# Performance work log

Measured on AMD Instinct MI355X. Metric: run time of the kernel, lower is better.

## Reference

```python
import jax, jax.numpy as jnp
import numpy as np

N_NODES = 100000
N_EDGES = 1600000
D = 64
HID = 512
N_CLASSES = 393


def gcn_conv(x, src, dst, W, b):
    """PyG-style GCNConv: h = x W; add self-loops; symmetric deg^-1/2 norm; scatter-add."""
    n = x.shape[0]
    h = x @ W  # [N, out]
    loop = jnp.arange(n)
    s = jnp.concatenate([src, loop])
    d = jnp.concatenate([dst, loop])
    deg = jax.ops.segment_sum(jnp.ones(d.shape[0], dtype=h.dtype), d, num_segments=n)
    dinv = jax.lax.rsqrt(jnp.maximum(deg, 1.0))  # self-loops guarantee deg >= 1
    norm = dinv[s] * dinv[d]  # [E+N]
    msg = h[s] * norm[:, None]  # [E+N, out] gather + scale
    out = jax.ops.segment_sum(msg, d, num_segments=n)  # scatter-add
    return out + b


def setup_inputs() -> dict:
    key = jax.random.key(0)
    ks = jax.random.split(key, 10)
    sc = 1.0 / np.sqrt(D)
    inp = {
        "adj": jax.random.randint(ks[0], (2, N_EDGES), 0, N_NODES, dtype=jnp.int64),
        "features": jax.random.normal(ks[1], (N_NODES, D), dtype=jnp.float32),
        "W1": jax.random.normal(ks[2], (D, D), dtype=jnp.float32) * sc,
        "b1": jnp.zeros((D,), jnp.float32),
        "W2": jax.random.normal(ks[3], (D, D), dtype=jnp.float32) * sc,
        "b2": jnp.zeros((D,), jnp.float32),
        "W3": jax.random.normal(ks[4], (D, D), dtype=jnp.float32) * sc,
        "b3": jnp.zeros((D,), jnp.float32),
        "Wlin": jax.random.normal(ks[5], (D, D), dtype=jnp.float32) * sc,
        "blin": jnp.zeros((D,), jnp.float32),
        "W4": jax.random.normal(ks[6], (N_NODES, HID), dtype=jnp.float32) / np.sqrt(N_NODES),
        "b4": jnp.zeros((HID,), jnp.float32),
        "W5": jax.random.normal(ks[7], (HID, N_CLASSES), dtype=jnp.float32) / np.sqrt(HID),
        "b5": jnp.zeros((N_CLASSES,), jnp.float32),
    }
    return inp


def reference(adj, features, W1, b1, W2, b2, W3, b3, Wlin, blin, W4, b4, W5, b5):
    src, dst = adj[0], adj[1]
    h = jax.nn.relu(gcn_conv(features, src, dst, W1, b1))
    h = jax.nn.relu(gcn_conv(h, src, dst, W2, b2))
    h = jax.nn.relu(gcn_conv(h, src, dst, W3, b3))
    scores = h @ Wlin + blin          # [N, 64]
    scores = scores.T                 # [64, N]
    scores = jax.nn.relu(scores @ W4 + b4)  # [64, HID]
    scores = scores @ W5 + b5         # [64, n_classes]
    return jax.nn.log_softmax(scores, axis=1)
```

## Files before the change

### kernel.cpp

```cpp
#include <hip/hip_runtime.h>
#include <math.h>

#define NN 100000
#define NE 1600000
#define HID 512
#define NCLS 393

__global__ void k_init(int* __restrict__ cnt, int* __restrict__ gtot) {
    int i = blockIdx.x * 256 + threadIdx.x;
    if (i < NN) cnt[i] = 0;
    if (i == 0) *gtot = 0;
}

__global__ void k_count(const int* __restrict__ dst, int* __restrict__ cnt) {
    int e = blockIdx.x * 256 + threadIdx.x;
    if (e < NE) atomicAdd(&cnt[dst[e]], 1);
}

__global__ void k_off(const int* __restrict__ cnt, float* __restrict__ dinv,
                      int* __restrict__ off, int* __restrict__ cur, int* __restrict__ gtot) {
    int i = blockIdx.x * 256 + threadIdx.x;
    if (i < NN) {
        int c = cnt[i];
        dinv[i] = rsqrtf(1.0f + (float)c);
        off[i] = atomicAdd(gtot, c);
        cur[i] = 0;
    }
}

__global__ void k_fill(const int* __restrict__ src, const int* __restrict__ dst,
                       const float* __restrict__ dinv, const int* __restrict__ off,
                       int* __restrict__ cur, int* __restrict__ eidx, float* __restrict__ enorm) {
    int e = blockIdx.x * 256 + threadIdx.x;
    if (e < NE) {
        int s = src[e], d = dst[e];
        int pos = off[d] + atomicAdd(&cur[d], 1);
        eidx[pos] = s;
        enorm[pos] = dinv[s] * dinv[d];
    }
}

template<bool IN_ACT, bool OUT_BIAS>
__global__ void k_gemm64b(const float* __restrict__ x, const float* __restrict__ W,
                          const float* __restrict__ bin, const float* __restrict__ bout,
                          float* __restrict__ out) {
    __shared__ float Ws[64 * 64];
    __shared__ float xs[32 * 64];
    int tid = threadIdx.x;
    size_t n0 = (size_t)blockIdx.x * 32;
    for (int i = tid; i < 1024; i += 256)
        ((float4*)Ws)[i] = ((const float4*)W)[i];
    for (int i = tid; i < 512; i += 256) {
        float4 v = ((const float4*)(x + n0 * 64))[i];
        if (IN_ACT) {
            int c = (i & 15) * 4;
            float4 bv = *(const float4*)(bin + c);
            v.x = fmaxf(v.x + bv.x, 0.f);
            v.y = fmaxf(v.y + bv.y, 0.f);
            v.z = fmaxf(v.z + bv.z, 0.f);
            v.w = fmaxf(v.w + bv.w, 0.f);
        }
        ((float4*)xs)[i] = v;
    }
    __syncthreads();
    int j = tid & 63, q = tid >> 6;
    float Wreg[64];
#pragma unroll
    for (int k = 0; k < 64; ++k) Wreg[k] = Ws[k * 64 + j];
    float bo = OUT_BIAS ? bout[j] : 0.f;
    for (int r = 0; r < 8; ++r) {
        int row = q * 8 + r;
        float acc = bo;
        const float4* xr = (const float4*)(xs + row * 64);
#pragma unroll
        for (int k4 = 0; k4 < 16; ++k4) {
            float4 xv = xr[k4];
            acc = fmaf(xv.x, Wreg[k4 * 4 + 0], acc);
            acc = fmaf(xv.y, Wreg[k4 * 4 + 1], acc);
            acc = fmaf(xv.z, Wreg[k4 * 4 + 2], acc);
            acc = fmaf(xv.w, Wreg[k4 * 4 + 3], acc);
        }
        out[(n0 + row) * 64 + j] = acc;
    }
}

__global__ void k_gather(const int* __restrict__ eidx, const float* __restrict__ enorm,
                         const int* __restrict__ off, const int* __restrict__ cnt,
                         const float* __restrict__ dinv, const float* __restrict__ t,
                         float* __restrict__ out) {
    int lane = threadIdx.x & 63;
    int n = (blockIdx.x * 256 + threadIdx.x) >> 6;
    if (n >= NN) return;
    float dv = dinv[n];
    float acc = t[(size_t)n * 64 + lane] * dv * dv;
    int o = off[n], c = cnt[n];
    for (int b = 0; b < c; b += 64) {
        int m = min(64, c - b);
        int sIdx = 0;
        float nrm = 0.f;
        if (lane < m) {
            sIdx = eidx[o + b + lane];
            nrm = enorm[o + b + lane];
        }
        int e = 0;
        for (; e + 4 <= m; e += 4) {
            int s0 = __shfl(sIdx, e + 0); float w0 = __shfl(nrm, e + 0);
            int s1 = __shfl(sIdx, e + 1); float w1 = __shfl(nrm, e + 1);
            int s2 = __shfl(sIdx, e + 2); float w2 = __shfl(nrm, e + 2);
            int s3 = __shfl(sIdx, e + 3); float w3 = __shfl(nrm, e + 3);
            float v0 = t[(size_t)s0 * 64 + lane];
            float v1 = t[(size_t)s1 * 64 + lane];
            float v2 = t[(size_t)s2 * 64 + lane];
            float v3 = t[(size_t)s3 * 64 + lane];
            acc = fmaf(v0, w0, acc);
            acc = fmaf(v1, w1, acc);
            acc = fmaf(v2, w2, acc);
            acc = fmaf(v3, w3, acc);
        }
        for (; e < m; ++e) {
            int s0 = __shfl(sIdx, e); float w0 = __shfl(nrm, e);
            acc = fmaf(t[(size_t)s0 * 64 + lane], w0, acc);
        }
    }
    out[(size_t)n * 64 + lane] = acc;
}

__global__ void k_zero(float* __restrict__ p, int n) {
    int i = blockIdx.x * 256 + threadIdx.x;
    if (i < n) p[i] = 0.f;
}

#define TG_KCHUNK 384
#define TG_NCH ((NN + TG_KCHUNK - 1) / TG_KCHUNK)
__global__ void k_tgemm2(const float* __restrict__ scores, const float* __restrict__ W4,
                         float* __restrict__ P) {
    __shared__ float ss[64 * 64];
    int colT = blockIdx.x & 3;
    int kch = blockIdx.x >> 2;
    int tid = threadIdx.x;
    int tc = tid & 31, tr = tid >> 5;
    int col = colT * 128 + tc * 4;
    float acc[8][4];
#pragma unroll
    for (int i = 0; i < 8; ++i)
#pragma unroll
        for (int c = 0; c < 4; ++c) acc[i][c] = 0.f;
    int k0 = kch * TG_KCHUNK;
    int k1 = min(k0 + TG_KCHUNK, NN);
    for (int kb = k0; kb < k1; kb += 64) {
        int cnt = min(64, k1 - kb);
        __syncthreads();
        for (int i = tid; i < 1024; i += 256) {
            float4 v = {0.f, 0.f, 0.f, 0.f};
            if ((i >> 4) < cnt) v = ((const float4*)(scores + (size_t)kb * 64))[i];
            ((float4*)ss)[i] = v;
        }
        __syncthreads();
        const float4* w4p = (const float4*)(W4 + (size_t)kb * 512 + col);
        for (int nIt = 0; nIt < cnt; ++nIt) {
            float4 w = w4p[(size_t)nIt * 128];
            const float4* sp = (const float4*)(ss + nIt * 64 + tr * 8);
            float4 s0 = sp[0], s1 = sp[1];
            float sarr[8] = {s0.x, s0.y, s0.z, s0.w, s1.x, s1.y, s1.z, s1.w};
#pragma unroll
            for (int i = 0; i < 8; ++i) {
                acc[i][0] = fmaf(sarr[i], w.x, acc[i][0]);
                acc[i][1] = fmaf(sarr[i], w.y, acc[i][1]);
                acc[i][2] = fmaf(sarr[i], w.z, acc[i][2]);
                acc[i][3] = fmaf(sarr[i], w.w, acc[i][3]);
            }
        }
    }
#pragma unroll
    for (int i = 0; i < 8; ++i) {
        int row = tr * 8 + i;
#pragma unroll
        for (int c = 0; c < 4; ++c)
            atomicAdd(&P[row * 512 + col + c], acc[i][c]);
    }
}

__global__ void k_final(const float* __restrict__ P, const float* __restrict__ b4,
                        const float* __restrict__ W5, const float* __restrict__ b5,
                        float* __restrict__ out) {
    __shared__ float p[HID];
    __shared__ float z[NCLS];
    __shared__ float red[256];
    int i = blockIdx.x;
    int tid = threadIdx.x;
    for (int k = tid; k < HID; k += 256) p[k] = fmaxf(P[i * HID + k] + b4[k], 0.f);
    __syncthreads();
    for (int c = tid; c < NCLS; c += 256) {
        float acc = b5[c];
        for (int k = 0; k < HID; ++k) acc = fmaf(p[k], W5[(size_t)k * NCLS + c], acc);
        z[c] = acc;
    }
    __syncthreads();
    float m = -INFINITY;
    for (int c = tid; c < NCLS; c += 256) m = fmaxf(m, z[c]);
    red[tid] = m;
    __syncthreads();
    for (int s = 128; s > 0; s >>= 1) {
        if (tid < s) red[tid] = fmaxf(red[tid], red[tid + s]);
        __syncthreads();
    }
    m = red[0];
    __syncthreads();
    float sum = 0.f;
    for (int c = tid; c < NCLS; c += 256) sum += expf(z[c] - m);
    red[tid] = sum;
    __syncthreads();
    for (int s = 128; s > 0; s >>= 1) {
        if (tid < s) red[tid] += red[tid + s];
        __syncthreads();
    }
    float lse = m + logf(red[0]);
    for (int c = tid; c < NCLS; c += 256) out[i * NCLS + c] = z[c] - lse;
}

extern "C" void kernel_launch(void* const* d_in, const int* in_sizes, int n_in,
                              void* d_out, int out_size, void* d_ws, size_t ws_size,
                              hipStream_t stream) {
    const int* adj = (const int*)d_in[0];
    const int* src = adj;
    const int* dst = adj + NE;
    const float* feat = (const float*)d_in[1];
    const float* W1 = (const float*)d_in[2];
    const float* b1 = (const float*)d_in[3];
    const float* W2 = (const float*)d_in[4];
    const float* b2 = (const float*)d_in[5];
    const float* W3 = (const float*)d_in[6];
    const float* b3 = (const float*)d_in[7];
    const float* Wlin = (const float*)d_in[8];
    const float* blin = (const float*)d_in[9];
    const float* W4 = (const float*)d_in[10];
    const float* b4 = (const float*)d_in[11];
    const float* W5 = (const float*)d_in[12];
    const float* b5 = (const float*)d_in[13];
    float* out = (float*)d_out;

    char* ws = (char*)d_ws;
    float* dinv = (float*)ws;                     ws += (size_t)NN * 4;
    int* cnt    = (int*)ws;                       ws += (size_t)NN * 4;
    int* off    = (int*)ws;                       ws += (size_t)NN * 4;
    int* cur    = (int*)ws;                       ws += (size_t)NN * 4;
    int* gtot   = (int*)ws;                       ws += 16;
    int* eidx   = (int*)ws;                       ws += (size_t)NE * 4;
    float* enorm= (float*)ws;                     ws += (size_t)NE * 4;
    float* bufA = (float*)ws;                     ws += (size_t)NN * 64 * 4;
    float* bufB = (float*)ws;                     ws += (size_t)NN * 64 * 4;
    float* P    = (float*)ws;                     ws += 64 * HID * 4;

    const int NB_N = (NN + 255) / 256;
    const int NB_E = NE / 256;
    const int NB_G = NN / 32;
    const int NB_GA = NN / 4;
    const int NB_T = 4 * TG_NCH;

    k_init<<<NB_N, 256, 0, stream>>>(cnt, gtot);
    k_count<<<NB_E, 256, 0, stream>>>(dst, cnt);
    k_off<<<NB_N, 256, 0, stream>>>(cnt, dinv, off, cur, gtot);
    k_fill<<<NB_E, 256, 0, stream>>>(src, dst, dinv, off, cur, eidx, enorm);

    k_gemm64b<false, false><<<NB_G, 256, 0, stream>>>(feat, W1, nullptr, nullptr, bufA);
    k_gather<<<NB_GA, 256, 0, stream>>>(eidx, enorm, off, cnt, dinv, bufA, bufB);
    k_gemm64b<true, false><<<NB_G, 256, 0, stream>>>(bufB, W2, b1, nullptr, bufA);
    k_gather<<<NB_GA, 256, 0, stream>>>(eidx, enorm, off, cnt, dinv, bufA, bufB);
    k_gemm64b<true, false><<<NB_G, 256, 0, stream>>>(bufB, W3, b2, nullptr, bufA);
    k_gather<<<NB_GA, 256, 0, stream>>>(eidx, enorm, off, cnt, dinv, bufA, bufB);
    k_gemm64b<true, true><<<NB_G, 256, 0, stream>>>(bufB, Wlin, b3, blin, bufA);

    k_zero<<<(64 * HID + 255) / 256, 256, 0, stream>>>(P, 64 * HID);
    k_tgemm2<<<NB_T, 256, 0, stream>>>(bufA, W4, P);

    k_final<<<64, 256, 0, stream>>>(P, b4, W5, b5, out);
}
```

Measured before the change: 1.074 ms.

## Pack edge index and norm, vectorize gather, split-K tgemm with separate reduce

Edge source index and norm now share one int2 array, so each neighbor costs one 8-byte load instead of two. The gather assigns 16 lanes per edge with float4 row loads, handling 4 edges per wave step, then combines the four partial sums with xor shuffles. The transposed GEMM writes per-chunk partials (192 chunks) into the spare bufB and sums them in a dedicated reduce kernel, replacing float atomics and the zero kernel. The reduce adds a pass over about 25 MB of partials, and the gather leaves lanes idle on the last iteration when a node's degree is not a multiple of 4.

Measured after the change: 958.9 us. 10.7% less time.

```diff
diff --git a/kernel.cpp b/kernel.cpp
--- a/kernel.cpp
+++ b/kernel.cpp
@@ -30,13 +30,12 @@
 
 __global__ void k_fill(const int* __restrict__ src, const int* __restrict__ dst,
                        const float* __restrict__ dinv, const int* __restrict__ off,
-                       int* __restrict__ cur, int* __restrict__ eidx, float* __restrict__ enorm) {
+                       int* __restrict__ cur, int2* __restrict__ epack) {
     int e = blockIdx.x * 256 + threadIdx.x;
     if (e < NE) {
         int s = src[e], d = dst[e];
         int pos = off[d] + atomicAdd(&cur[d], 1);
-        eidx[pos] = s;
-        enorm[pos] = dinv[s] * dinv[d];
+        epack[pos] = make_int2(s, __float_as_int(dinv[s] * dinv[d]));
     }
 }
 
@@ -84,59 +83,51 @@
     }
 }
 
-__global__ void k_gather(const int* __restrict__ eidx, const float* __restrict__ enorm,
-                         const int* __restrict__ off, const int* __restrict__ cnt,
-                         const float* __restrict__ dinv, const float* __restrict__ t,
-                         float* __restrict__ out) {
+__global__ void k_gather2(const int2* __restrict__ epack, const int* __restrict__ off,
+                          const int* __restrict__ cnt, const float* __restrict__ dinv,
+                          const float* __restrict__ t, float* __restrict__ out) {
     int lane = threadIdx.x & 63;
     int n = (blockIdx.x * 256 + threadIdx.x) >> 6;
     if (n >= NN) return;
-    float dv = dinv[n];
-    float acc = t[(size_t)n * 64 + lane] * dv * dv;
+    int g = lane >> 4, f4 = lane & 15;
     int o = off[n], c = cnt[n];
-    for (int b = 0; b < c; b += 64) {
-        int m = min(64, c - b);
-        int sIdx = 0;
-        float nrm = 0.f;
-        if (lane < m) {
-            sIdx = eidx[o + b + lane];
-            nrm = enorm[o + b + lane];
-        }
-        int e = 0;
-        for (; e + 4 <= m; e += 4) {
-            int s0 = __shfl(sIdx, e + 0); float w0 = __shfl(nrm, e + 0);
-            int s1 = __shfl(sIdx, e + 1); float w1 = __shfl(nrm, e + 1);
-            int s2 = __shfl(sIdx, e + 2); float w2 = __shfl(nrm, e + 2);
-            int s3 = __shfl(sIdx, e + 3); float w3 = __shfl(nrm, e + 3);
-            float v0 = t[(size_t)s0 * 64 + lane];
-            float v1 = t[(size_t)s1 * 64 + lane];
-            float v2 = t[(size_t)s2 * 64 + lane];
-            float v3 = t[(size_t)s3 * 64 + lane];
-            acc = fmaf(v0, w0, acc);
-            acc = fmaf(v1, w1, acc);
-            acc = fmaf(v2, w2, acc);
-            acc = fmaf(v3, w3, acc);
-        }
-        for (; e < m; ++e) {
-            int s0 = __shfl(sIdx, e); float w0 = __shfl(nrm, e);
-            acc = fmaf(t[(size_t)s0 * 64 + lane], w0, acc);
-        }
-    }
-    out[(size_t)n * 64 + lane] = acc;
-}
-
-__global__ void k_zero(float* __restrict__ p, int n) {
-    int i = blockIdx.x * 256 + threadIdx.x;
-    if (i < n) p[i] = 0.f;
-}
-
-#define TG_KCHUNK 384
-#define TG_NCH ((NN + TG_KCHUNK - 1) / TG_KCHUNK)
-__global__ void k_tgemm2(const float* __restrict__ scores, const float* __restrict__ W4,
-                         float* __restrict__ P) {
+    float ax = 0.f, ay = 0.f, az = 0.f, aw = 0.f;
+    for (int b = 0; b < c; b += 4) {
+        int idx = b + g;
+        if (idx < c) {
+            int2 ep = epack[o + idx];
+            float w = __int_as_float(ep.y);
+            float4 v = *(const float4*)(t + (size_t)ep.x * 64 + f4 * 4);
+            ax = fmaf(v.x, w, ax);
+            ay = fmaf(v.y, w, ay);
+            az = fmaf(v.z, w, az);
+            aw = fmaf(v.w, w, aw);
+        }
+    }
+    ax += __shfl_xor(ax, 16); ay += __shfl_xor(ay, 16);
+    az += __shfl_xor(az, 16); aw += __shfl_xor(aw, 16);
+    ax += __shfl_xor(ax, 32); ay += __shfl_xor(ay, 32);
+    az += __shfl_xor(az, 32); aw += __shfl_xor(aw, 32);
+    if (lane < 16) {
+        float dv = dinv[n];
+        float d2 = dv * dv;
+        float4 self = *(const float4*)(t + (size_t)n * 64 + f4 * 4);
+        float4 r;
+        r.x = ax + self.x * d2;
+        r.y = ay + self.y * d2;
+        r.z = az + self.z * d2;
+        r.w = aw + self.w * d2;
+        *(float4*)(out + (size_t)n * 64 + f4 * 4) = r;
+    }
+}
+
+#define TG_SPLIT 192
+#define TG_CHUNK 521
+__global__ void k_tgemm3(const float* __restrict__ scores, const float* __restrict__ W4,
+                         float* __restrict__ Pp) {
     __shared__ float ss[64 * 64];
     int colT = blockIdx.x & 3;
-    int kch = blockIdx.x >> 2;
+    int kc = blockIdx.x >> 2;
     int tid = threadIdx.x;
     int tc = tid & 31, tr = tid >> 5;
     int col = colT * 128 + tc * 4;
@@ -145,8 +136,8 @@
     for (int i = 0; i < 8; ++i)
 #pragma unroll
         for (int c = 0; c < 4; ++c) acc[i][c] = 0.f;
-    int k0 = kch * TG_KCHUNK;
-    int k1 = min(k0 + TG_KCHUNK, NN);
+    int k0 = kc * TG_CHUNK;
+    int k1 = min(k0 + TG_CHUNK, NN);
     for (int kb = k0; kb < k1; kb += 64) {
         int cnt = min(64, k1 - kb);
         __syncthreads();
@@ -156,28 +147,39 @@
             ((float4*)ss)[i] = v;
         }
         __syncthreads();
-        const float4* w4p = (const float4*)(W4 + (size_t)kb * 512 + col);
+        const float* w4base = W4 + (size_t)kb * 512 + col;
         for (int nIt = 0; nIt < cnt; ++nIt) {
-            float4 w = w4p[(size_t)nIt * 128];
+            float4 w = *(const float4*)(w4base + (size_t)nIt * 512);
             const float4* sp = (const float4*)(ss + nIt * 64 + tr * 8);
             float4 s0 = sp[0], s1 = sp[1];
-            float sarr[8] = {s0.x, s0.y, s0.z, s0.w, s1.x, s1.y, s1.z, s1.w};
+            float sa[8] = {s0.x, s0.y, s0.z, s0.w, s1.x, s1.y, s1.z, s1.w};
 #pragma unroll
             for (int i = 0; i < 8; ++i) {
-                acc[i][0] = fmaf(sarr[i], w.x, acc[i][0]);
-                acc[i][1] = fmaf(sarr[i], w.y, acc[i][1]);
-                acc[i][2] = fmaf(sarr[i], w.z, acc[i][2]);
-                acc[i][3] = fmaf(sarr[i], w.w, acc[i][3]);
+                acc[i][0] = fmaf(sa[i], w.x, acc[i][0]);
+                acc[i][1] = fmaf(sa[i], w.y, acc[i][1]);
+                acc[i][2] = fmaf(sa[i], w.z, acc[i][2]);
+                acc[i][3] = fmaf(sa[i], w.w, acc[i][3]);
             }
         }
     }
+    float* pb = Pp + (size_t)kc * 64 * 512;
 #pragma unroll
     for (int i = 0; i < 8; ++i) {
         int row = tr * 8 + i;
-#pragma unroll
-        for (int c = 0; c < 4; ++c)
-            atomicAdd(&P[row * 512 + col + c], acc[i][c]);
-    }
+        *(float4*)(pb + row * 512 + col) = make_float4(acc[i][0], acc[i][1], acc[i][2], acc[i][3]);
+    }
+}
+
+__global__ void k_reduce(const float* __restrict__ Pp, float* __restrict__ P) {
+    int i = blockIdx.x * 256 + threadIdx.x;
+    float s0 = 0.f, s1 = 0.f, s2 = 0.f, s3 = 0.f;
+    for (int kc = 0; kc < TG_SPLIT; kc += 4) {
+        s0 += Pp[(size_t)(kc + 0) * 32768 + i];
+        s1 += Pp[(size_t)(kc + 1) * 32768 + i];
+        s2 += Pp[(size_t)(kc + 2) * 32768 + i];
+        s3 += Pp[(size_t)(kc + 3) * 32768 + i];
+    }
+    P[i] = (s0 + s1) + (s2 + s3);
 }
 
 __global__ void k_final(const float* __restrict__ P, const float* __restrict__ b4,
@@ -240,38 +242,38 @@
     float* out = (float*)d_out;
 
     char* ws = (char*)d_ws;
-    float* dinv = (float*)ws;                     ws += (size_t)NN * 4;
-    int* cnt    = (int*)ws;                       ws += (size_t)NN * 4;
-    int* off    = (int*)ws;                       ws += (size_t)NN * 4;
-    int* cur    = (int*)ws;                       ws += (size_t)NN * 4;
-    int* gtot   = (int*)ws;                       ws += 16;
-    int* eidx   = (int*)ws;                       ws += (size_t)NE * 4;
-    float* enorm= (float*)ws;                     ws += (size_t)NE * 4;
-    float* bufA = (float*)ws;                     ws += (size_t)NN * 64 * 4;
-    float* bufB = (float*)ws;                     ws += (size_t)NN * 64 * 4;
-    float* P    = (float*)ws;                     ws += 64 * HID * 4;
+    float* dinv  = (float*)ws;  ws += (size_t)NN * 4;
+    int*   cnt   = (int*)ws;    ws += (size_t)NN * 4;
+    int*   off   = (int*)ws;    ws += (size_t)NN * 4;
+    int*   cur   = (int*)ws;    ws += (size_t)NN * 4;
+    int*   gtot  = (int*)ws;    ws += 16;
+    int2*  epack = (int2*)ws;   ws += (size_t)NE * 8;
+    float* bufA  = (float*)ws;  ws += (size_t)NN * 64 * 4;
+    float* bufB  = (float*)ws;  ws += (size_t)NN * 64 * 4;
+    float* P     = (float*)ws;  ws += 64 * HID * 4;
 
     const int NB_N = (NN + 255) / 256;
     const int NB_E = NE / 256;
     const int NB_G = NN / 32;
     const int NB_GA = NN / 4;
-    const int NB_T = 4 * TG_NCH;
+    const int NB_T = 4 * TG_SPLIT;
 
     k_init<<<NB_N, 256, 0, stream>>>(cnt, gtot);
     k_count<<<NB_E, 256, 0, stream>>>(dst, cnt);
     k_off<<<NB_N, 256, 0, stream>>>(cnt, dinv, off, cur, gtot);
-    k_fill<<<NB_E, 256, 0, stream>>>(src, dst, dinv, off, cur, eidx, enorm);
+    k_fill<<<NB_E, 256, 0, stream>>>(src, dst, dinv, off, cur, epack);
 
     k_gemm64b<false, false><<<NB_G, 256, 0, stream>>>(feat, W1, nullptr, nullptr, bufA);
-    k_gather<<<NB_GA, 256, 0, stream>>>(eidx, enorm, off, cnt, dinv, bufA, bufB);
+    k_gather2<<<NB_GA, 256, 0, stream>>>(epack, off, cnt, dinv, bufA, bufB);
     k_gemm64b<true, false><<<NB_G, 256, 0, stream>>>(bufB, W2, b1, nullptr, bufA);
-    k_gather<<<NB_GA, 256, 0, stream>>>(eidx, enorm, off, cnt, dinv, bufA, bufB);
+    k_gather2<<<NB_GA, 256, 0, stream>>>(epack, off, cnt, dinv, bufA, bufB);
     k_gemm64b<true, false><<<NB_G, 256, 0, stream>>>(bufB, W3, b2, nullptr, bufA);
-    k_gather<<<NB_GA, 256, 0, stream>>>(eidx, enorm, off, cnt, dinv, bufA, bufB);
+    k_gather2<<<NB_GA, 256, 0, stream>>>(epack, off, cnt, dinv, bufA, bufB);
     k_gemm64b<true, true><<<NB_G, 256, 0, stream>>>(bufB, Wlin, b3, blin, bufA);
 
-    k_zero<<<(64 * HID + 255) / 256, 256, 0, stream>>>(P, 64 * HID);
-    k_tgemm2<<<NB_T, 256, 0, stream>>>(bufA, W4, P);
+    float* Pp = bufB;
+    k_tgemm3<<<NB_T, 256, 0, stream>>>(bufA, W4, Pp);
+    k_reduce<<<(64 * HID) / 256, 256, 0, stream>>>(Pp, P);
 
     k_final<<<64, 256, 0, stream>>>(P, b4, W5, b5, out);
 }
```
